# Kernel optimization log

Hardware: AMD Instinct MI355X
Metric: run time of the kernel (lower is better)

Reference implementation:

```python
import jax, jax.numpy as jnp
import numpy as np

D_MODEL = 64
NHEAD = 4
DK = D_MODEL // NHEAD  # 16
MODES1 = 12
MODES2 = 12
IM = (64, 64)  # (full_H, W)
SIGMA = 5.0


def _gauss_flat():
    # Faithful to torch gaussian_2d_kernel: meshgrid(arange(W), arange(H), 'ij') -> shape (W, H)
    gx, gy = jnp.meshgrid(jnp.arange(IM[1], dtype=jnp.float32),
                          jnp.arange(IM[0], dtype=jnp.float32), indexing='ij')
    cH = (IM[0] - 1) / 2.0
    cW = (IM[1] - 1) / 2.0
    k = jnp.exp(-0.5 * ((gx - cW) ** 2 + (gy - cH) ** 2) / (SIGMA ** 2))
    return (k / k.sum()).reshape(-1)  # flattened (W*H,) == (H*W,) numerically used flat


def _spectral(x, w):
    # x: [B,T,H,W,C] ; w: [2(weights1/2), 2(re/im), C, DK, MODES1, MODES2, NHEAD]
    xp = jnp.transpose(x, (0, 1, 4, 2, 3))  # [B,T,C,H,W]
    B, T, C, H, W = xp.shape
    xft = jnp.fft.rfft2(xp)  # [B,T,C,H,W//2+1] complex64
    W1 = w[0, 0] + 1j * w[0, 1]
    W2 = w[1, 0] + 1j * w[1, 1]
    lo = jnp.einsum('bnixy,ioxyh->bnoxyh', xft[:, :, :, :MODES1, :MODES2], W1)
    hi = jnp.einsum('bnixy,ioxyh->bnoxyh', xft[:, :, :, H - MODES1:, :MODES2], W2)
    out_ft = jnp.zeros((B, T, DK, H, W // 2 + 1, NHEAD), dtype=lo.dtype)
    out_ft = out_ft.at[:, :, :, :MODES1, :MODES2, :].set(lo)
    out_ft = out_ft.at[:, :, :, H - MODES1:, :MODES2, :].set(hi)
    o = jnp.fft.irfft2(out_ft, s=(H, W), axes=(-3, -2))  # [B,T,DK,H,W,NHEAD]
    return jnp.transpose(o, (0, 1, 3, 4, 2, 5))  # [B,T,H,W,DK,NHEAD]


def setup_inputs() -> dict:
    key = jax.random.key(0)
    ks = jax.random.split(key, 5)
    z = jax.random.normal(ks[0], (4, 32, 64, 64, 64), dtype=jnp.float32)
    scale = 1.0 / (D_MODEL * DK)
    wshape = (2, 2, D_MODEL, DK, MODES1, MODES2, NHEAD)
    return {
        'z': z,
        'wq': scale * jax.random.uniform(ks[1], wshape, dtype=jnp.float32),
        'wk': scale * jax.random.uniform(ks[2], wshape, dtype=jnp.float32),
        'wvx': scale * jax.random.uniform(ks[3], wshape, dtype=jnp.float32),
        'wvy': scale * jax.random.uniform(ks[4], wshape, dtype=jnp.float32),
    }


def reference(z, wq, wk, wvx, wvy):
    B, T, fH, W, _ = z.shape
    H = fH // 2
    x, y = z[:, :, :H], z[:, :, H:]
    hf = lambda a: jnp.transpose(a, (0, 5, 1, 2, 3, 4))  # -> [B,nH,T,H,W,dk]
    q = hf(_spectral(x, wq))
    k = hf(_spectral(x, wk))
    vx = hf(_spectral(x, wvx))
    vy = hf(_spectral(y, wvy))
    v = jnp.concatenate([vx, vy], axis=3)  # [B,nH,T,fH,W,dk]
    scale = float(IM[0] * IM[1])  # sqrt((H*W)^2)
    qf = q.reshape(B, NHEAD, T, -1)
    kf = k.reshape(B, NHEAD, T, -1)
    scores = jnp.einsum('bntc,bnsc->bnts', qf, kf) / scale  # [B,nH,T,T]
    # Original materializes scores[...,None,None]*gauss -> [B,nH,T,T,H,W]; since the
    # Gaussian factor is separable we fuse: out[b,n,p,m,d] = g[m] * sum_q s[p,q] v[q,m,d]
    g = _gauss_flat()  # [fH*W]
    vf = v.reshape(B, NHEAD, T, fH * W, DK)
    out = jnp.einsum('bnpq,bnqmd->bnpmd', scores, vf) * g[None, None, None, :, None]
    # raw contiguous reshape, exactly as torch .view + .reshape
    return out.reshape(B, T, fH, W, -1)
```

## Files before the change

### kernel.cpp

```cpp
#include <hip/hip_runtime.h>
#include <math.h>

#define PI2 6.283185307179586f

#define SZ_U  (128ull*64*12*64*2)
#define OFF_X (SZ_U)
#define SZ_Q  (4ull*4*32*288*16*2)
#define DO_WP (4ull*SZ_Q)
#define DO_P  (DO_WP + 9437184ull)
#define DO_S  (DO_P + 786432ull)
#define C0f   5.9604644775390625e-8f

__global__ __launch_bounds__(256) void k0_repack(
    const float* __restrict__ wq, const float* __restrict__ wk,
    const float* __restrict__ wvx, const float* __restrict__ wvy,
    float* __restrict__ dout) {
  const float* src = (blockIdx.y==0)?wq:(blockIdx.y==1)?wk:(blockIdx.y==2)?wvx:wvy;
  float* wp = dout + DO_WP;
  int base = (blockIdx.x*256 + threadIdx.x)*4;
  #pragma unroll
  for (int u=0; u<4; ++u) {
    int s4 = base + u;
    int m2 = s4 % 12;  int r1 = s4/12;
    int m1 = r1 % 12;  int r2 = r1/12;
    int o  = r2 % 16;  int r3 = r2/16;
    int i  = r3 & 63;  int r4 = r3 >> 6;
    int ri = r4 & 1;   int p  = r4 >> 1;
    int j  = (p*12 + m1)*12 + m2;
    float4 v = ((const float4*)src)[s4];
    size_t d4 = ((size_t)(blockIdx.y*288 + j)*2 + ri)*1024 + (size_t)i*16 + o;
    ((float4*)wp)[d4] = v;
  }
}

__global__ __launch_bounds__(256) void k1a_dftw(const float* __restrict__ z, float* __restrict__ ws) {
  float* U = ws;
  int tid = threadIdx.x;
  int c4 = tid & 15, kg = (tid>>4)&3, rsub = tid>>6;
  int bt = blockIdx.x >> 3, rg = blockIdx.x & 7;
  float ck[3], sk[3];
  #pragma unroll
  for (int kk=0; kk<3; ++kk) { float s,c; sincosf((PI2/64.f)*(kg+4*kk), &s, &c); ck[kk]=c; sk[kk]=s; }
  for (int it=0; it<2; ++it) {
    int r = rg*8 + it*4 + rsub;
    const float4* zr = (const float4*)(z + ((size_t)bt*64 + r)*4096) + c4;
    float ar[3][4]={{0}}, ai[3][4]={{0}};
    float tr[3]={1.f,1.f,1.f}, ti[3]={0.f,0.f,0.f};
    #pragma unroll 8
    for (int w=0; w<64; ++w) {
      float4 x = zr[(size_t)w*16];
      #pragma unroll
      for (int kk=0; kk<3; ++kk) {
        ar[kk][0] += x.x*tr[kk]; ai[kk][0] += x.x*ti[kk];
        ar[kk][1] += x.y*tr[kk]; ai[kk][1] += x.y*ti[kk];
        ar[kk][2] += x.z*tr[kk]; ai[kk][2] += x.z*ti[kk];
        ar[kk][3] += x.w*tr[kk]; ai[kk][3] += x.w*ti[kk];
        float nr = tr[kk]*ck[kk] + ti[kk]*sk[kk];
        float ni = ti[kk]*ck[kk] - tr[kk]*sk[kk];
        tr[kk]=nr; ti[kk]=ni;
      }
    }
    #pragma unroll
    for (int kk=0; kk<3; ++kk) {
      int kw = kg+4*kk;
      float4* up = (float4*)(U + (((size_t)bt*64 + r)*12 + kw)*128 + c4*8);
      up[0] = make_float4(ar[kk][0],ai[kk][0],ar[kk][1],ai[kk][1]);
      up[1] = make_float4(ar[kk][2],ai[kk][2],ar[kk][3],ai[kk][3]);
    }
  }
}

__global__ __launch_bounds__(256) void k1b_dfth(float* __restrict__ ws) {
  const float* U = ws;
  float* X = ws + OFF_X;
  __shared__ float Et[768*2];
  __shared__ float Ut[32*192*2];
  int tid = threadIdx.x;
  for (int q = tid; q < 768; q += 256) {
    int h = q/24, ki = q%24;
    int kh = ki<12 ? ki : ki+8;
    float s,c; sincosf((PI2/32.f)*((kh*h)&31), &s, &c);
    Et[q*2] = c; Et[q*2+1] = -s;
  }
  int bt = blockIdx.x>>3, half = (blockIdx.x>>2)&1, c0 = (blockIdx.x&3)*16;
  for (int q = tid; q < 6144; q += 256) {
    int h = q/192, col = q%192, kw = col>>4, cc = col&15;
    ((float2*)Ut)[q] = *((const float2*)(U + (((size_t)bt*64 + half*32 + h)*12 + kw)*128) + (c0+cc));
  }
  __syncthreads();
  int k3 = tid>>5, cg = tid&31;
  float vr[3][6]={{0}}, vi[3][6]={{0}};
  for (int h=0; h<32; ++h) {
    float er[3], ei[3];
    #pragma unroll
    for (int a=0;a<3;a++){ int ki=k3*3+a; er[a]=Et[(h*24+ki)*2]; ei[a]=Et[(h*24+ki)*2+1]; }
    #pragma unroll
    for (int k=0;k<6;k++){
      float2 u = *(float2*)&Ut[(h*192 + cg + 32*k)*2];
      #pragma unroll
      for (int a=0;a<3;a++){
        vr[a][k] += u.x*er[a] - u.y*ei[a];
        vi[a][k] += u.y*er[a] + u.x*ei[a];
      }
    }
  }
  #pragma unroll
  for (int a=0;a<3;a++)
    #pragma unroll
    for (int k=0;k<6;k++){
      int col = cg+32*k, kw = col>>4, cc = col&15, ki = k3*3+a, j = ki*12+kw;
      *(float2*)(X + ((size_t)(bt*2+half)*288 + j)*128 + (size_t)(c0+cc)*2) = make_float2(vr[a][k], vi[a][k]);
    }
}

__global__ __launch_bounds__(256,3) void k2_wmul(const float* __restrict__ ws, float* __restrict__ dout) {
  const float* X = ws + OFF_X;
  const float* Wp = dout + DO_WP;
  __shared__ float Xs[64*132];
  __shared__ float Ws[32*128];
  int j = blockIdx.x, half = blockIdx.y, btc = blockIdx.z;
  int tid = threadIdx.x;
  for (int q = tid; q < 2048; q += 256) {
    int btL = q>>5, c4 = q&31;
    float4 v = *((const float4*)(X + ((size_t)((btc*64+btL)*2 + half)*288 + j)*128) + c4);
    *(float4*)&Xs[btL*132 + c4*4] = v;
  }
  int nt = (half==0) ? 3 : 1, tb = (half==0) ? 0 : 3;
  int trow = tid>>4, tcol = tid&15;
  for (int it=0; it<nt; ++it) {
    int tau = tb + it;
    const float4* wsrc = (const float4*)(Wp + ((size_t)(tau*288 + j))*8192);
    float ar[4][4]={{0}}, ai[4][4]={{0}};
    for (int kh=0; kh<2; ++kh) {
      __syncthreads();
      for (int q = tid; q < 512; q += 256) {
        float4 a = wsrc[kh*512 + q];
        float4 b = wsrc[1024 + kh*512 + q];
        int i32 = q>>4, o = q&15;
        float* wd = &Ws[i32*128 + o*2];
        *(float2*)&wd[0]  = make_float2(a.x, b.x);
        *(float2*)&wd[32] = make_float2(a.y, b.y);
        *(float2*)&wd[64] = make_float2(a.z, b.z);
        *(float2*)&wd[96] = make_float2(a.w, b.w);
      }
      __syncthreads();
      const float* xb = &Xs[trow*132 + kh*64];
      const float* wb = &Ws[tcol*2];
      #pragma unroll 8
      for (int i=0; i<32; ++i) {
        float xr[4], xi[4], wr[4], wi[4];
        #pragma unroll
        for (int a=0;a<4;a++){
          float2 xv = *(const float2*)&xb[a*2112 + i*2];
          xr[a]=xv.x; xi[a]=xv.y;
        }
        #pragma unroll
        for (int b=0;b<4;b++){
          float2 wv = *(const float2*)&wb[i*128 + b*32];
          wr[b]=wv.x; wi[b]=wv.y;
        }
        #pragma unroll
        for (int a=0;a<4;a++)
          #pragma unroll
          for (int b=0;b<4;b++){
            ar[a][b] += xr[a]*wr[b] - xi[a]*wi[b];
            ai[a][b] += xr[a]*wi[b] + xi[a]*wr[b];
          }
      }
    }
    float* obase = dout + (size_t)tau*SZ_Q;
    #pragma unroll
    for (int a=0;a<4;a++){
      int bt = btc*64 + trow + 16*a;
      int b_ = bt>>5, t = bt&31;
      #pragma unroll
      for (int bb=0;bb<4;bb++){
        int o = tcol, n = bb;
        *(float2*)(obase + ((((size_t)(b_*4+n)*32 + t)*288 + j)*16 + o)*2) = make_float2(ar[a][bb], ai[a][bb]);
      }
    }
  }
}

__global__ __launch_bounds__(256) void k3_scores(float* __restrict__ dout) {
  const float* Q = dout;
  const float* K = dout + SZ_Q;
  float* P = dout + DO_P;
  __shared__ float lds[12544];
  float* Qs = lds;
  float* Ks = lds + 6272;
  int jc = blockIdx.x, bn = blockIdx.y;
  int tid = threadIdx.x;
  for (int q = tid; q < 1536; q += 256) {
    int t = q/48, f4 = q%48;
    *(float4*)&Qs[t*196 + f4*4] = *((const float4*)(Q + (size_t)(bn*32+t)*9216 + jc*192) + f4);
  }
  for (int q = tid; q < 1536; q += 256) {
    int s = q/48, f4 = q%48;
    int kw = (jc*6 + (f4>>3)) % 12;
    float w1 = (kw==0) ? C0f : 4.f*C0f;
    float4 v = *((const float4*)(K + (size_t)(bn*32+s)*9216 + jc*192) + f4);
    v.x*=w1; v.y*=w1; v.z*=w1; v.w*=w1;
    *(float4*)&Ks[s*196 + f4*4] = v;
  }
  __syncthreads();
  if (((jc&1)==0) && ((jc>>1)!=12)) {
    int khI = jc>>1;
    int jp = ((24 - khI) % 24) * 12;
    for (int q = tid; q < 512; q += 256) {
      int s = q>>4, d = q&15;
      float2 kp = *((const float2*)(K + (size_t)(bn*32+s)*9216 + (size_t)jp*32) + d);
      Ks[s*196 + d*2]     += C0f * kp.x;
      Ks[s*196 + d*2 + 1] -= C0f * kp.y;
    }
  }
  __syncthreads();
  int tq = tid>>5, sq = (tid>>2)&7, eg = tid&3;
  float acc[4][4]={{0}};
  for (int e=0; e<12; ++e) {
    float4 qv[4], kv[4];
    #pragma unroll
    for (int a=0;a<4;a++) qv[a] = *(float4*)&Qs[(tq*4+a)*196 + eg*48 + e*4];
    #pragma unroll
    for (int b=0;b<4;b++) kv[b] = *(float4*)&Ks[(sq*4+b)*196 + eg*48 + e*4];
    #pragma unroll
    for (int a=0;a<4;a++)
      #pragma unroll
      for (int b=0;b<4;b++)
        acc[a][b] += qv[a].x*kv[b].x + qv[a].y*kv[b].y + qv[a].z*kv[b].z + qv[a].w*kv[b].w;
  }
  __syncthreads();
  float* Pp = lds;
  #pragma unroll
  for (int a=0;a<4;a++)
    #pragma unroll
    for (int b=0;b<4;b++)
      Pp[eg*1056 + (tq*4+a)*33 + (sq*4+b)] = acc[a][b];
  __syncthreads();
  for (int q = tid; q < 1024; q += 256) {
    int t = q>>5, s = q&31;
    float r = Pp[t*33+s] + Pp[1056 + t*33+s] + Pp[2112 + t*33+s] + Pp[3168 + t*33+s];
    P[(size_t)(jc*16 + bn)*1024 + q] = r;
  }
}

__global__ __launch_bounds__(256) void k3b_reduce(float* __restrict__ dout) {
  const float* P = dout + DO_P;
  float* S = dout + DO_S;
  int bn = blockIdx.x, tid = threadIdx.x;
  for (int q = tid; q < 1024; q += 256) {
    float a = 0.f;
    for (int jc=0; jc<48; ++jc) a += P[(size_t)(jc*16+bn)*1024 + q];
    S[bn*1024 + q] = a;
  }
}

__global__ __launch_bounds__(256) void k4_mix(const float* __restrict__ dout, float* __restrict__ ws) {
  const float* S = dout + DO_S;
  const float* V = dout + (blockIdx.z==0 ? 2ull*SZ_Q : 3ull*SZ_Q);
  float* O = ws + (blockIdx.z==0 ? 0ull : SZ_Q);
  __shared__ float scs[1056];
  __shared__ float Vs[32*388];
  int jc = blockIdx.x, bn = blockIdx.y, tid = threadIdx.x;
  for (int q = tid; q < 1024; q += 256) scs[(q>>5)*33 + (q&31)] = S[bn*1024 + q];
  for (int q = tid; q < 3072; q += 256) {
    int s = q/96, f4 = q%96;
    *(float4*)&Vs[s*388 + f4*4] = *((const float4*)(V + (size_t)(bn*32+s)*9216 + jc*384) + f4);
  }
  __syncthreads();
  int tq = tid>>5, ec = tid&31;
  float4 acc[4][3];
  #pragma unroll
  for (int a=0;a<4;a++)
    #pragma unroll
    for (int c=0;c<3;c++) acc[a][c] = make_float4(0.f,0.f,0.f,0.f);
  for (int s=0; s<32; ++s) {
    float sc[4];
    #pragma unroll
    for (int a=0;a<4;a++) sc[a] = scs[(tq*4+a)*33 + s];
    #pragma unroll
    for (int cc=0;cc<3;cc++){
      float4 v = *(float4*)&Vs[s*388 + (ec+32*cc)*4];
      #pragma unroll
      for (int a=0;a<4;a++){
        acc[a][cc].x += sc[a]*v.x; acc[a][cc].y += sc[a]*v.y;
        acc[a][cc].z += sc[a]*v.z; acc[a][cc].w += sc[a]*v.w;
      }
    }
  }
  #pragma unroll
  for (int a=0;a<4;a++)
    #pragma unroll
    for (int cc=0;cc<3;cc++)
      *((float4*)(O + (size_t)(bn*32 + tq*4+a)*9216 + jc*384) + (ec+32*cc)) = acc[a][cc];
}

__global__ __launch_bounds__(512) void k5_out(const float* __restrict__ ws, float* __restrict__ dout) {
  __shared__ float Cs[6144];
  __shared__ float gt[64];
  int tid = threadIdx.x;
  int idx  = blockIdx.x;
  int half = blockIdx.y;
  int rnd  = blockIdx.z;
  if (tid < 64) { float dr = tid - 31.5f; gt[tid] = expf(-0.02f*dr*dr); }
  __syncthreads();
  float gsum = 0.f;
  for (int i=0;i<64;i++) gsum += gt[i];
  const float* src = ws + (half ? SZ_Q : 0ull) + (size_t)idx*9216;
  {
    int h2 = tid>>6, cg = tid&63;
    int h0 = rnd*16 + h2*2, h1 = h0+1;
    float s0,c0s,s1,c1s;
    sincosf((PI2/32.f)*h0, &s0, &c0s);
    sincosf((PI2/32.f)*h1, &s1, &c1s);
    float e0r=1.f, e0i=0.f, e1r=1.f, e1i=0.f;
    float a0r[3]={0},a0i[3]={0},a1r[3]={0},a1i[3]={0};
    const float2* sp = (const float2*)src;
    for (int ki=0; ki<24; ++ki) {
      if (ki==12) {
        float s,c;
        sincosf((PI2/32.f)*((20*h0)&31), &s, &c); e0r=c; e0i=s;
        sincosf((PI2/32.f)*((20*h1)&31), &s, &c); e1r=c; e1i=s;
      }
      #pragma unroll
      for (int k=0;k<3;k++){
        float2 f = sp[ki*192 + cg + 64*k];
        a0r[k] += f.x*e0r - f.y*e0i;  a0i[k] += f.x*e0i + f.y*e0r;
        a1r[k] += f.x*e1r - f.y*e1i;  a1i[k] += f.x*e1i + f.y*e1r;
      }
      float n0r = e0r*c0s - e0i*s0, n0i = e0r*s0 + e0i*c0s; e0r=n0r; e0i=n0i;
      float n1r = e1r*c1s - e1i*s1, n1i = e1r*s1 + e1i*c1s; e1r=n1r; e1i=n1i;
    }
    #pragma unroll
    for (int k=0;k<3;k++){
      int col = cg+64*k, kw = col>>4;
      float sc = (kw==0 ? 1.f : 2.f) * (1.f/2048.f);
      int base0 = (h2*2*192 + col)*2;
      Cs[base0]     = a0r[k]*sc; Cs[base0+1]   = a0i[k]*sc;
      Cs[base0+384] = a1r[k]*sc; Cs[base0+385] = a1i[k]*sc;
    }
  }
  __syncthreads();
  {
    int hl = tid>>5, wg = (tid>>2)&7, dq = tid&3;
    float cr[12][4], ci[12][4];
    #pragma unroll
    for (int kw=0;kw<12;kw++){
      float4 u = *(float4*)&Cs[hl*384 + kw*32 + dq*8];
      float4 v = *(float4*)&Cs[hl*384 + kw*32 + dq*8 + 4];
      cr[kw][0]=u.x; ci[kw][0]=u.y; cr[kw][1]=u.z; ci[kw][1]=u.w;
      cr[kw][2]=v.x; ci[kw][2]=v.y; cr[kw][3]=v.z; ci[kw][3]=v.w;
    }
    int row = half*32 + rnd*16 + hl;
    float grow = gt[row]/gsum;
    float pr, pi;
    sincosf((PI2/64.f)*wg, &pi, &pr);
    float* ob = dout + (size_t)idx*65536 + (size_t)row*1024;
    for (int k=0;k<8;k++){
      int w = wg + 8*k;
      float v0=cr[0][0], v1=cr[0][1], v2=cr[0][2], v3=cr[0][3];
      float tr=pr, ti=pi;
      #pragma unroll
      for (int kw=1;kw<12;kw++){
        v0 += cr[kw][0]*tr - ci[kw][0]*ti;
        v1 += cr[kw][1]*tr - ci[kw][1]*ti;
        v2 += cr[kw][2]*tr - ci[kw][2]*ti;
        v3 += cr[kw][3]*tr - ci[kw][3]*ti;
        float nr = tr*pr - ti*pi, ni = tr*pi + ti*pr;
        tr=nr; ti=ni;
      }
      float g = grow * (gt[w]/gsum);
      *(float4*)(ob + w*16 + dq*4) = make_float4(v0*g, v1*g, v2*g, v3*g);
      float nr = (pr - pi)*0.70710678118654752f;
      float ni = (pr + pi)*0.70710678118654752f;
      pr=nr; pi=ni;
    }
  }
}

extern "C" void kernel_launch(void* const* d_in, const int* in_sizes, int n_in,
                              void* d_out, int out_size, void* d_ws, size_t ws_size,
                              hipStream_t stream) {
  const float* z   = (const float*)d_in[0];
  const float* wq  = (const float*)d_in[1];
  const float* wk  = (const float*)d_in[2];
  const float* wvx = (const float*)d_in[3];
  const float* wvy = (const float*)d_in[4];
  float* out = (float*)d_out;
  float* ws  = (float*)d_ws;
  hipLaunchKernelGGL(k0_repack, dim3(576,4), dim3(256), 0, stream, wq, wk, wvx, wvy, out);
  hipLaunchKernelGGL(k1a_dftw,  dim3(1024),  dim3(256), 0, stream, z, ws);
  hipLaunchKernelGGL(k1b_dfth,  dim3(1024),  dim3(256), 0, stream, ws);
  hipLaunchKernelGGL(k2_wmul,   dim3(288,2,2), dim3(256), 0, stream, ws, out);
  hipLaunchKernelGGL(k3_scores, dim3(48,16), dim3(256), 0, stream, out);
  hipLaunchKernelGGL(k3b_reduce,dim3(16),    dim3(256), 0, stream, out);
  hipLaunchKernelGGL(k4_mix,    dim3(24,16,2), dim3(256), 0, stream, out, ws);
  hipLaunchKernelGGL(k5_out,    dim3(512,2,2), dim3(512), 0, stream, ws, out);
}
```

Measured before the change: 574.4 us.

## Split k2 weight-multiply grid per projection and prefetch weight halves into registers

The k2_wmul grid now gives each projection (q, k, vx, vy) its own block along y, instead of having half-0 blocks loop over three projections. This balances the load and doubles the block count. The weight tiles for both K-halves are loaded into registers early, so the global load of the second half overlaps the first half's compute. As a cost, the shared X tile is reloaded once per projection rather than reused across three, and register pressure rises.

```diff
diff --git a/kernel.cpp b/kernel.cpp
--- a/kernel.cpp
+++ b/kernel.cpp
@@ -118,66 +118,103 @@
   const float* Wp = dout + DO_WP;
   __shared__ float Xs[64*132];
   __shared__ float Ws[32*128];
-  int j = blockIdx.x, half = blockIdx.y, btc = blockIdx.z;
+  int j = blockIdx.x, tau = blockIdx.y, btc = blockIdx.z;
+  int half = (tau==3) ? 1 : 0;
   int tid = threadIdx.x;
+  const float4* wsrc = (const float4*)(Wp + ((size_t)(tau*288 + j))*8192);
+  float4 wa0[2], wb0[2];
+  #pragma unroll
+  for (int u=0;u<2;++u){ wa0[u]=wsrc[tid+256*u]; wb0[u]=wsrc[1024+tid+256*u]; }
   for (int q = tid; q < 2048; q += 256) {
     int btL = q>>5, c4 = q&31;
     float4 v = *((const float4*)(X + ((size_t)((btc*64+btL)*2 + half)*288 + j)*128) + c4);
     *(float4*)&Xs[btL*132 + c4*4] = v;
   }
-  int nt = (half==0) ? 3 : 1, tb = (half==0) ? 0 : 3;
+  #pragma unroll
+  for (int u=0;u<2;++u){
+    int q = tid+256*u; int i32 = q>>4, o = q&15;
+    float* wd = &Ws[i32*128 + o*2];
+    *(float2*)&wd[0]  = make_float2(wa0[u].x, wb0[u].x);
+    *(float2*)&wd[32] = make_float2(wa0[u].y, wb0[u].y);
+    *(float2*)&wd[64] = make_float2(wa0[u].z, wb0[u].z);
+    *(float2*)&wd[96] = make_float2(wa0[u].w, wb0[u].w);
+  }
+  float4 wa1[2], wb1[2];
+  #pragma unroll
+  for (int u=0;u<2;++u){ wa1[u]=wsrc[512+tid+256*u]; wb1[u]=wsrc[1536+tid+256*u]; }
   int trow = tid>>4, tcol = tid&15;
-  for (int it=0; it<nt; ++it) {
-    int tau = tb + it;
-    const float4* wsrc = (const float4*)(Wp + ((size_t)(tau*288 + j))*8192);
-    float ar[4][4]={{0}}, ai[4][4]={{0}};
-    for (int kh=0; kh<2; ++kh) {
-      __syncthreads();
-      for (int q = tid; q < 512; q += 256) {
-        float4 a = wsrc[kh*512 + q];
-        float4 b = wsrc[1024 + kh*512 + q];
-        int i32 = q>>4, o = q&15;
-        float* wd = &Ws[i32*128 + o*2];
-        *(float2*)&wd[0]  = make_float2(a.x, b.x);
-        *(float2*)&wd[32] = make_float2(a.y, b.y);
-        *(float2*)&wd[64] = make_float2(a.z, b.z);
-        *(float2*)&wd[96] = make_float2(a.w, b.w);
-      }
-      __syncthreads();
-      const float* xb = &Xs[trow*132 + kh*64];
-      const float* wb = &Ws[tcol*2];
-      #pragma unroll 8
-      for (int i=0; i<32; ++i) {
-        float xr[4], xi[4], wr[4], wi[4];
-        #pragma unroll
-        for (int a=0;a<4;a++){
-          float2 xv = *(const float2*)&xb[a*2112 + i*2];
-          xr[a]=xv.x; xi[a]=xv.y;
-        }
+  float ar[4][4]={{0}}, ai[4][4]={{0}};
+  __syncthreads();
+  {
+    const float* xb = &Xs[trow*132];
+    const float* wb = &Ws[tcol*2];
+    #pragma unroll 8
+    for (int i=0; i<32; ++i) {
+      float xr[4], xi[4], wr[4], wi[4];
+      #pragma unroll
+      for (int a=0;a<4;a++){
+        float2 xv = *(const float2*)&xb[a*2112 + i*2];
+        xr[a]=xv.x; xi[a]=xv.y;
+      }
+      #pragma unroll
+      for (int b=0;b<4;b++){
+        float2 wv = *(const float2*)&wb[i*128 + b*32];
+        wr[b]=wv.x; wi[b]=wv.y;
+      }
+      #pragma unroll
+      for (int a=0;a<4;a++)
         #pragma unroll
         for (int b=0;b<4;b++){
-          float2 wv = *(const float2*)&wb[i*128 + b*32];
-          wr[b]=wv.x; wi[b]=wv.y;
+          ar[a][b] += xr[a]*wr[b] - xi[a]*wi[b];
+          ai[a][b] += xr[a]*wi[b] + xi[a]*wr[b];
         }
+    }
+  }
+  __syncthreads();
+  #pragma unroll
+  for (int u=0;u<2;++u){
+    int q = tid+256*u; int i32 = q>>4, o = q&15;
+    float* wd = &Ws[i32*128 + o*2];
+    *(float2*)&wd[0]  = make_float2(wa1[u].x, wb1[u].x);
+    *(float2*)&wd[32] = make_float2(wa1[u].y, wb1[u].y);
+    *(float2*)&wd[64] = make_float2(wa1[u].z, wb1[u].z);
+    *(float2*)&wd[96] = make_float2(wa1[u].w, wb1[u].w);
+  }
+  __syncthreads();
+  {
+    const float* xb = &Xs[trow*132 + 64];
+    const float* wb = &Ws[tcol*2];
+    #pragma unroll 8
+    for (int i=0; i<32; ++i) {
+      float xr[4], xi[4], wr[4], wi[4];
+      #pragma unroll
+      for (int a=0;a<4;a++){
+        float2 xv = *(const float2*)&xb[a*2112 + i*2];
+        xr[a]=xv.x; xi[a]=xv.y;
+      }
+      #pragma unroll
+      for (int b=0;b<4;b++){
+        float2 wv = *(const float2*)&wb[i*128 + b*32];
+        wr[b]=wv.x; wi[b]=wv.y;
+      }
+      #pragma unroll
+      for (int a=0;a<4;a++)
         #pragma unroll
-        for (int a=0;a<4;a++)
-          #pragma unroll
-          for (int b=0;b<4;b++){
-            ar[a][b] += xr[a]*wr[b] - xi[a]*wi[b];
-            ai[a][b] += xr[a]*wi[b] + xi[a]*wr[b];
-          }
-      }
-    }
-    float* obase = dout + (size_t)tau*SZ_Q;
-    #pragma unroll
-    for (int a=0;a<4;a++){
-      int bt = btc*64 + trow + 16*a;
-      int b_ = bt>>5, t = bt&31;
-      #pragma unroll
-      for (int bb=0;bb<4;bb++){
-        int o = tcol, n = bb;
-        *(float2*)(obase + ((((size_t)(b_*4+n)*32 + t)*288 + j)*16 + o)*2) = make_float2(ar[a][bb], ai[a][bb]);
-      }
+        for (int b=0;b<4;b++){
+          ar[a][b] += xr[a]*wr[b] - xi[a]*wi[b];
+          ai[a][b] += xr[a]*wi[b] + xi[a]*wr[b];
+        }
+    }
+  }
+  float* obase = dout + (size_t)tau*SZ_Q;
+  #pragma unroll
+  for (int a=0;a<4;a++){
+    int bt = btc*64 + trow + 16*a;
+    int b_ = bt>>5, t = bt&31;
+    #pragma unroll
+    for (int bb=0;bb<4;bb++){
+      int o = tcol, n = bb;
+      *(float2*)(obase + ((((size_t)(b_*4+n)*32 + t)*288 + j)*16 + o)*2) = make_float2(ar[a][bb], ai[a][bb]);
     }
   }
 }
@@ -391,7 +428,7 @@
   hipLaunchKernelGGL(k0_repack, dim3(576,4), dim3(256), 0, stream, wq, wk, wvx, wvy, out);
   hipLaunchKernelGGL(k1a_dftw,  dim3(1024),  dim3(256), 0, stream, z, ws);
   hipLaunchKernelGGL(k1b_dfth,  dim3(1024),  dim3(256), 0, stream, ws);
-  hipLaunchKernelGGL(k2_wmul,   dim3(288,2,2), dim3(256), 0, stream, ws, out);
+  hipLaunchKernelGGL(k2_wmul,   dim3(288,4,2), dim3(256), 0, stream, ws, out);
   hipLaunchKernelGGL(k3_scores, dim3(48,16), dim3(256), 0, stream, out);
   hipLaunchKernelGGL(k3b_reduce,dim3(16),    dim3(256), 0, stream, out);
   hipLaunchKernelGGL(k4_mix,    dim3(24,16,2), dim3(256), 0, stream, out, ws);
```

New measurement: 578.0 us. No clear change (+0.6%).
